# Performance work log

Hardware: AMD Instinct MI355X
Metric: run time of the kernel (lower is better)

## Reference

```python
import jax, jax.numpy as jnp
import numpy as np

HIDDEN = 1024
HEADS = 16
HEAD_DIM = HIDDEN // HEADS  # 64
BLOCK = 1024  # block_size; seq_len > BLOCK triggers ring path
B, S = 1, 4096


def setup_inputs() -> dict:
    key = jax.random.key(0)
    k0, k1, k2, k3, k4 = jax.random.split(key, 5)
    w_scale = 0.02
    return {
        "hidden_states": jax.random.normal(k0, (B, S, HIDDEN), dtype=jnp.float32),
        # weights stored [in, out]; applied as x @ W (equivalent to nn.Linear with W.T)
        "w_q": jax.random.normal(k1, (HIDDEN, HIDDEN), dtype=jnp.float32) * w_scale,
        "w_k": jax.random.normal(k2, (HIDDEN, HIDDEN), dtype=jnp.float32) * w_scale,
        "w_v": jax.random.normal(k3, (HIDDEN, HIDDEN), dtype=jnp.float32) * w_scale,
        "w_o": jax.random.normal(k4, (HIDDEN, HIDDEN), dtype=jnp.float32) * w_scale,
    }


def _ring_attention(q, k, v, block, scale):
    # q,k,v: [B, H, S, D]. Faithful to the torch module: each KV block subtracts
    # its OWN local max (no running-max rescale); exp-sums and weighted-V are
    # accumulated additively across KV blocks, then normalized once at the end.
    b, h, s, d = q.shape
    nb = s // block
    kb = jnp.moveaxis(k.reshape(b, h, nb, block, d), 2, 0)  # [nb, B, H, block, D]
    vb = jnp.moveaxis(v.reshape(b, h, nb, block, d), 2, 0)

    def step(carry, kv):
        num, den = carry
        k_blk, v_blk = kv
        s_blk = jnp.einsum("bhqd,bhkd->bhqk", q, k_blk) * scale  # [B,H,S,block]
        m = jnp.max(s_blk, axis=-1, keepdims=True)               # local max only
        e = jnp.exp(s_blk - m)
        num = num + jnp.einsum("bhqk,bhkd->bhqd", e, v_blk)
        den = den + jnp.sum(e, axis=-1, keepdims=True)
        return (num, den), None

    init = (jnp.zeros_like(q), jnp.zeros((b, h, s, 1), dtype=q.dtype))
    (num, den), _ = jax.lax.scan(step, init, (kb, vb))
    return num / den


def reference(hidden_states, w_q, w_k, w_v, w_o):
    b, s, _ = hidden_states.shape
    q = (hidden_states @ w_q).reshape(b, s, HEADS, HEAD_DIM).transpose(0, 2, 1, 3)
    k = (hidden_states @ w_k).reshape(b, s, HEADS, HEAD_DIM).transpose(0, 2, 1, 3)
    v = (hidden_states @ w_v).reshape(b, s, HEADS, HEAD_DIM).transpose(0, 2, 1, 3)
    scale = HEAD_DIM ** -0.5
    out = _ring_attention(q, k, v, BLOCK, scale)          # [B,H,S,D]
    out = out.transpose(0, 2, 1, 3).reshape(b, s, HIDDEN)  # [B,S,hidden]
    return out @ w_o
```

## Files before the change

kernel.cpp:

```cpp
#include <hip/hip_runtime.h>
#include <hip/hip_bf16.h>

typedef __bf16 bf16;
typedef bf16 bf16x2 __attribute__((ext_vector_type(2)));
typedef bf16 bf16x4 __attribute__((ext_vector_type(4)));
typedef bf16 bf16x8 __attribute__((ext_vector_type(8)));
typedef float f32x4 __attribute__((ext_vector_type(4)));

#define HID 1024
#define NHEADS 16
#define HD 64
#define SEQ 4096

__device__ __forceinline__ void gll16(const void* g, void* l) {
  __builtin_amdgcn_global_load_lds(
      (const __attribute__((address_space(1))) void*)g,
      (__attribute__((address_space(3))) void*)l, 16, 0, 0);
}

__global__ __launch_bounds__(256)
void prep_kernel(const float* __restrict__ X,
                 const float* __restrict__ Wq, const float* __restrict__ Wk,
                 const float* __restrict__ Wv, const float* __restrict__ Wo,
                 bf16* __restrict__ Xb, bf16* __restrict__ Wt)
{
  const int z = blockIdx.z, t = threadIdx.x, bx = blockIdx.x;
  if (z == 0) {
    const float4* src = (const float4*)X;
    const int gid = bx * 256 + t;
    #pragma unroll
    for (int i = 0; i < 16; ++i) {
      float4 v = src[gid + i * 65536];
      bf16x4 o = {(bf16)v.x, (bf16)v.y, (bf16)v.z, (bf16)v.w};
      *(bf16x4*)&Xb[(size_t)(gid + i * 65536) * 4] = o;
    }
  } else {
    const float* W = (z == 1) ? Wq : (z == 2) ? Wk : (z == 3) ? Wv : Wo;
    bf16* dst = Wt + (size_t)(z - 1) * HID * HID;
    const float scale = (z == 1) ? 0.125f : 1.0f;
    __shared__ bf16 T[64][68];
    const int tr = (bx >> 4) * 64, tc = (bx & 15) * 64;
    #pragma unroll
    for (int p = 0; p < 4; ++p) {
      int row = (t >> 4) + p * 16;
      float4 v = *(const float4*)&W[(size_t)(tr + row) * HID + tc + (t & 15) * 4];
      T[row][(t & 15) * 4 + 0] = (bf16)(v.x * scale);
      T[row][(t & 15) * 4 + 1] = (bf16)(v.y * scale);
      T[row][(t & 15) * 4 + 2] = (bf16)(v.z * scale);
      T[row][(t & 15) * 4 + 3] = (bf16)(v.w * scale);
    }
    __syncthreads();
    #pragma unroll
    for (int p = 0; p < 4; ++p) {
      int rp = (t >> 4) + p * 16;
      int cb = (t & 15) * 4;
      bf16x4 o = {T[cb + 0][rp], T[cb + 1][rp], T[cb + 2][rp], T[cb + 3][rp]};
      *(bf16x4*)&dst[(size_t)(tc + rp) * HID + tr + cb] = o;
    }
  }
}

__global__ __launch_bounds__(256)
void qkv_gemm(const bf16* __restrict__ A, const bf16* __restrict__ Wt,
              bf16* __restrict__ Qg, bf16* __restrict__ Kg,
              bf16* __restrict__ Vt)
{
  __shared__ bf16 sbuf[16384];
  bf16* As = sbuf;
  bf16* Bs = sbuf + 8192;

  const int t = threadIdx.x, lane = t & 63, w = t >> 6;
  const int z = blockIdx.z;
  const int n0 = blockIdx.x * 128, m0 = blockIdx.y * 128;
  const bf16* Bt = Wt + (size_t)z * HID * HID;
  const int wm = (w & 1) * 64, wn = (w >> 1) * 64;
  const int fr = lane & 15, quad = lane >> 4;

  f32x4 acc[4][4] = {};

  const int sr = lane >> 3;
  const int sc = ((lane & 7) - sr) & 7;
  const bf16* ga = A  + (size_t)(m0 + w * 32 + sr) * HID + sc * 8;
  const bf16* gb = Bt + (size_t)(n0 + w * 32 + sr) * HID + sc * 8;

  for (int k0 = 0; k0 < HID; k0 += 64) {
    __syncthreads();
    #pragma unroll
    for (int c = 0; c < 4; ++c) {
      gll16(ga + (size_t)(c * 8) * HID + k0, As + (w * 32 + c * 8) * 64);
      gll16(gb + (size_t)(c * 8) * HID + k0, Bs + (w * 32 + c * 8) * 64);
    }
    __syncthreads();
    #pragma unroll
    for (int ks = 0; ks < 2; ++ks) {
      bf16x8 af[4], bg[4];
      #pragma unroll
      for (int i = 0; i < 4; ++i)
        af[i] = *(const bf16x8*)&As[(wm + i * 16 + fr) * 64 +
                                    ((ks * 4 + quad + fr) & 7) * 8];
      #pragma unroll
      for (int i = 0; i < 4; ++i)
        bg[i] = *(const bf16x8*)&Bs[(wn + i * 16 + fr) * 64 +
                                    ((ks * 4 + quad + fr) & 7) * 8];
      #pragma unroll
      for (int mi = 0; mi < 4; ++mi)
        #pragma unroll
        for (int ni = 0; ni < 4; ++ni)
          acc[mi][ni] = __builtin_amdgcn_mfma_f32_16x16x32_bf16(
              af[mi], bg[ni], acc[mi][ni], 0, 0, 0);
    }
  }

  if (z < 2) {
    bf16* C = z ? Kg : Qg;
    #pragma unroll
    for (int mi = 0; mi < 4; ++mi)
      #pragma unroll
      for (int ni = 0; ni < 4; ++ni)
        #pragma unroll
        for (int r = 0; r < 4; ++r)
          C[(size_t)(m0 + wm + mi * 16 + quad * 4 + r) * HID +
            n0 + wn + ni * 16 + fr] = (bf16)acc[mi][ni][r];
  } else {
    __syncthreads();
    #pragma unroll
    for (int mi = 0; mi < 4; ++mi)
      #pragma unroll
      for (int ni = 0; ni < 4; ++ni)
        #pragma unroll
        for (int r = 0; r < 4; ++r) {
          int row = wn + ni * 16 + fr;
          int col = wm + mi * 16 + quad * 4 + r;
          int colS = (col + 8 * (row & 15)) & 127;
          sbuf[row * 128 + colS] = (bf16)acc[mi][ni][r];
        }
    __syncthreads();
    const int row = t >> 1, cb = (t & 1) * 64;
    #pragma unroll
    for (int j = 0; j < 8; ++j) {
      int c0 = (cb + j * 8 + 8 * (row & 15)) & 127;
      *(bf16x8*)&Vt[(size_t)(n0 + row) * SEQ + m0 + cb + j * 8] =
          *(const bf16x8*)&sbuf[row * 128 + c0];
    }
  }
}

__global__ __launch_bounds__(256)
void oproj_gemm(const bf16* __restrict__ A, const bf16* __restrict__ Bt,
                float* __restrict__ C)
{
  __shared__ bf16 sbuf[16384];
  bf16* As = sbuf;
  bf16* Bs = sbuf + 8192;

  const int t = threadIdx.x, lane = t & 63, w = t >> 6;
  const int n0 = blockIdx.x * 128, m0 = blockIdx.y * 128;
  const int wm = (w & 1) * 64, wn = (w >> 1) * 64;
  const int fr = lane & 15, quad = lane >> 4;

  f32x4 acc[4][4] = {};

  const int sr = lane >> 3;
  const int sc = ((lane & 7) - sr) & 7;
  const bf16* ga = A  + (size_t)(m0 + w * 32 + sr) * HID + sc * 8;
  const bf16* gb = Bt + (size_t)(n0 + w * 32 + sr) * HID + sc * 8;

  for (int k0 = 0; k0 < HID; k0 += 64) {
    __syncthreads();
    #pragma unroll
    for (int c = 0; c < 4; ++c) {
      gll16(ga + (size_t)(c * 8) * HID + k0, As + (w * 32 + c * 8) * 64);
      gll16(gb + (size_t)(c * 8) * HID + k0, Bs + (w * 32 + c * 8) * 64);
    }
    __syncthreads();
    #pragma unroll
    for (int ks = 0; ks < 2; ++ks) {
      bf16x8 af[4], bg[4];
      #pragma unroll
      for (int i = 0; i < 4; ++i)
        af[i] = *(const bf16x8*)&As[(wm + i * 16 + fr) * 64 +
                                    ((ks * 4 + quad + fr) & 7) * 8];
      #pragma unroll
      for (int i = 0; i < 4; ++i)
        bg[i] = *(const bf16x8*)&Bs[(wn + i * 16 + fr) * 64 +
                                    ((ks * 4 + quad + fr) & 7) * 8];
      #pragma unroll
      for (int mi = 0; mi < 4; ++mi)
        #pragma unroll
        for (int ni = 0; ni < 4; ++ni)
          acc[mi][ni] = __builtin_amdgcn_mfma_f32_16x16x32_bf16(
              af[mi], bg[ni], acc[mi][ni], 0, 0, 0);
    }
  }

  #pragma unroll
  for (int mi = 0; mi < 4; ++mi)
    #pragma unroll
    for (int ni = 0; ni < 4; ++ni)
      #pragma unroll
      for (int r = 0; r < 4; ++r)
        C[(size_t)(m0 + wm + mi * 16 + quad * 4 + r) * HID +
          n0 + wn + ni * 16 + fr] = acc[mi][ni][r];
}

__global__ __launch_bounds__(256)
void attn3(const bf16* __restrict__ Q, const bf16* __restrict__ K,
           const bf16* __restrict__ Vt, bf16* __restrict__ O)
{
  __shared__ bf16 Ks[2][4096];
  __shared__ bf16 Vs[2][4096];
  __shared__ bf16 Ps[4][2048];

  const int t = threadIdx.x, lane = t & 63, w = t >> 6;
  const int h = blockIdx.y, q0 = blockIdx.x * 128;
  const int fr = lane & 15, quad = lane >> 4;

  bf16x8 bq[2][2];
  #pragma unroll
  for (int qf = 0; qf < 2; ++qf)
    #pragma unroll
    for (int ks = 0; ks < 2; ++ks)
      bq[qf][ks] = *(const bf16x8*)&Q[(size_t)(q0 + w * 32 + qf * 16 + fr) * HID
                                      + h * 64 + ks * 32 + quad * 8];

  const int sr = lane >> 3;
  const int sc = ((lane & 7) - sr) & 7;
  const bf16* gk = K  + (size_t)(w * 16 + sr) * HID + h * 64 + sc * 8;
  const bf16* gv = Vt + (size_t)(h * 64 + w * 16 + sr) * SEQ + sc * 8;

  #pragma unroll
  for (int j = 0; j < 2; ++j) {
    gll16(gk + (size_t)(j * 8) * HID, &Ks[0][(w * 16 + j * 8) * 64]);
    gll16(gv + (size_t)(j * 8) * SEQ, &Vs[0][(w * 16 + j * 8) * 64]);
  }

  f32x4 accN[2][4] = {};
  f32x4 accO[2][4] = {};
  float m_i[2] = {-3e38f, -3e38f}, l_i[2] = {0.f, 0.f}, den[2] = {0.f, 0.f};

  __syncthreads();

  for (int kk = 0; kk < 64; ++kk) {
    const int buf = kk & 1;
    if (kk < 63) {
      const size_t key0n = (size_t)(kk + 1) * 64;
      #pragma unroll
      for (int j = 0; j < 2; ++j) {
        gll16(gk + (key0n + j * 8) * HID, &Ks[buf ^ 1][(w * 16 + j * 8) * 64]);
        gll16(gv + key0n + (size_t)(j * 8) * SEQ,
              &Vs[buf ^ 1][(w * 16 + j * 8) * 64]);
      }
    }

    bf16x8 ak[4][2];
    #pragma unroll
    for (int mt = 0; mt < 4; ++mt)
      #pragma unroll
      for (int ks = 0; ks < 2; ++ks)
        ak[mt][ks] = *(const bf16x8*)&Ks[buf][(mt * 16 + fr) * 64 +
                                             ((ks * 4 + quad + fr) & 7) * 8];

    #pragma unroll
    for (int qf = 0; qf < 2; ++qf) {
      f32x4 s[4];
      #pragma unroll
      for (int mt = 0; mt < 4; ++mt) {
        f32x4 z = {};
        z = __builtin_amdgcn_mfma_f32_16x16x32_bf16(ak[mt][0], bq[qf][0], z, 0, 0, 0);
        z = __builtin_amdgcn_mfma_f32_16x16x32_bf16(ak[mt][1], bq[qf][1], z, 0, 0, 0);
        s[mt] = z;
      }
      float mx = -3e38f;
      #pragma unroll
      for (int mt = 0; mt < 4; ++mt)
        #pragma unroll
        for (int r = 0; r < 4; ++r) mx = fmaxf(mx, s[mt][r]);
      mx = fmaxf(mx, __shfl_xor(mx, 16));
      mx = fmaxf(mx, __shfl_xor(mx, 32));
      const float mnew = fmaxf(m_i[qf], mx);
      const float alpha = __expf(m_i[qf] - mnew);
      m_i[qf] = mnew;
      float sum = 0.f;
      const int prow = (qf * 16 + fr) * 64;
      #pragma unroll
      for (int mt = 0; mt < 4; ++mt) {
        float p0 = __expf(s[mt][0] - mnew);
        float p1 = __expf(s[mt][1] - mnew);
        float p2 = __expf(s[mt][2] - mnew);
        float p3 = __expf(s[mt][3] - mnew);
        sum += (p0 + p1) + (p2 + p3);
        bf16x4 pv = {(bf16)p0, (bf16)p1, (bf16)p2, (bf16)p3};
        *(bf16x4*)&Ps[w][prow + ((mt * 2 + (quad >> 1) + fr) & 7) * 8 +
                         (quad & 1) * 4] = pv;
      }
      sum += __shfl_xor(sum, 16);
      sum += __shfl_xor(sum, 32);
      l_i[qf] = l_i[qf] * alpha + sum;
      #pragma unroll
      for (int dt = 0; dt < 4; ++dt) accO[qf][dt] *= alpha;
    }

    #pragma unroll
    for (int ks = 0; ks < 2; ++ks) {
      bf16x8 bp0 = *(const bf16x8*)&Ps[w][fr * 64 +
                                          ((ks * 4 + quad + fr) & 7) * 8];
      bf16x8 bp1 = *(const bf16x8*)&Ps[w][(16 + fr) * 64 +
                                          ((ks * 4 + quad + fr) & 7) * 8];
      #pragma unroll
      for (int dt = 0; dt < 4; ++dt) {
        bf16x8 av = *(const bf16x8*)&Vs[buf][(dt * 16 + fr) * 64 +
                                            ((ks * 4 + quad + fr) & 7) * 8];
        accO[0][dt] = __builtin_amdgcn_mfma_f32_16x16x32_bf16(av, bp0, accO[0][dt], 0, 0, 0);
        accO[1][dt] = __builtin_amdgcn_mfma_f32_16x16x32_bf16(av, bp1, accO[1][dt], 0, 0, 0);
      }
    }

    if ((kk & 15) == 15) {
      #pragma unroll
      for (int qf = 0; qf < 2; ++qf) {
        #pragma unroll
        for (int dt = 0; dt < 4; ++dt) {
          #pragma unroll
          for (int r = 0; r < 4; ++r) accN[qf][dt][r] += accO[qf][dt][r];
          accO[qf][dt] = (f32x4){0.f, 0.f, 0.f, 0.f};
        }
        den[qf] += l_i[qf];
        l_i[qf] = 0.f;
        m_i[qf] = -3e38f;
      }
    }
    __syncthreads();
  }

  #pragma unroll
  for (int qf = 0; qf < 2; ++qf) {
    const float inv = 1.0f / den[qf];
    const size_t orow = (size_t)(q0 + w * 32 + qf * 16 + fr) * HID + h * 64;
    #pragma unroll
    for (int dt = 0; dt < 4; ++dt) {
      bf16x4 ov = {(bf16)(accN[qf][dt][0] * inv), (bf16)(accN[qf][dt][1] * inv),
                   (bf16)(accN[qf][dt][2] * inv), (bf16)(accN[qf][dt][3] * inv)};
      *(bf16x4*)&O[orow + dt * 16 + quad * 4] = ov;
    }
  }
}

extern "C" void kernel_launch(void* const* d_in, const int* in_sizes, int n_in,
                              void* d_out, int out_size, void* d_ws, size_t ws_size,
                              hipStream_t stream)
{
  const float* X  = (const float*)d_in[0];
  const float* Wq = (const float*)d_in[1];
  const float* Wk = (const float*)d_in[2];
  const float* Wv = (const float*)d_in[3];
  const float* Wo = (const float*)d_in[4];
  float* out = (float*)d_out;

  const size_t MB = 1024 * 1024;
  bf16* Xb  = (bf16*)d_ws;
  bf16* Wt  = (bf16*)((char*)d_ws + 8  * MB);
  bf16* Qg  = (bf16*)((char*)d_ws + 16 * MB);
  bf16* Kg  = (bf16*)((char*)d_ws + 24 * MB);
  bf16* Vtg = (bf16*)((char*)d_ws + 32 * MB);
  bf16* Og  = (bf16*)((char*)d_ws + 40 * MB);

  prep_kernel<<<dim3(256, 1, 5), 256, 0, stream>>>(X, Wq, Wk, Wv, Wo, Xb, Wt);
  qkv_gemm<<<dim3(HID / 128, SEQ / 128, 3), 256, 0, stream>>>(Xb, Wt, Qg, Kg, Vtg);
  attn3<<<dim3(SEQ / 128, NHEADS), 256, 0, stream>>>(Qg, Kg, Vtg, Og);
  oproj_gemm<<<dim3(HID / 128, SEQ / 128), 256, 0, stream>>>(
      Og, Wt + (size_t)3 * HID * HID, out);
}
```

Measured before the change: 274.9 us.

## Split attention KV blocks across grid z with atomic accumulation and normalize pass

Attention is split along the key dimension so each of four z-slices handles one 1024-key block. Partial numerators and denominators are accumulated into fp32 workspace with atomics and then normalized by a separate kernel. The aim is to raise the grid from 512 to 2048 workgroups to fill the GPU better. The cost is a memset, atomic traffic and an extra kernel launch. Double-buffered K/V loading is also replaced by a single buffer with two barriers per iteration, which removes load/compute overlap. Whether the split path runs depends on the workspace being at least 68 MB.

Result: slower. 428.2 us (+55.8%).

```diff
diff --git a/kernel.cpp b/kernel.cpp
--- a/kernel.cpp
+++ b/kernel.cpp
@@ -2,7 +2,6 @@
 #include <hip/hip_bf16.h>
 
 typedef __bf16 bf16;
-typedef bf16 bf16x2 __attribute__((ext_vector_type(2)));
 typedef bf16 bf16x4 __attribute__((ext_vector_type(4)));
 typedef bf16 bf16x8 __attribute__((ext_vector_type(8)));
 typedef float f32x4 __attribute__((ext_vector_type(4)));
@@ -203,16 +202,19 @@
           n0 + wn + ni * 16 + fr] = acc[mi][ni][r];
 }
 
+template <int NSPLIT>
 __global__ __launch_bounds__(256)
-void attn3(const bf16* __restrict__ Q, const bf16* __restrict__ K,
-           const bf16* __restrict__ Vt, bf16* __restrict__ O)
-{
-  __shared__ bf16 Ks[2][4096];
-  __shared__ bf16 Vs[2][4096];
+void attn4(const bf16* __restrict__ Q, const bf16* __restrict__ K,
+           const bf16* __restrict__ Vt, float* __restrict__ numg,
+           float* __restrict__ deng, bf16* __restrict__ Og)
+{
+  __shared__ bf16 Ks[4096];
+  __shared__ bf16 Vs[4096];
   __shared__ bf16 Ps[4][2048];
 
   const int t = threadIdx.x, lane = t & 63, w = t >> 6;
   const int h = blockIdx.y, q0 = blockIdx.x * 128;
+  const int z = blockIdx.z;
   const int fr = lane & 15, quad = lane >> 4;
 
   bf16x8 bq[2][2];
@@ -225,50 +227,44 @@
 
   const int sr = lane >> 3;
   const int sc = ((lane & 7) - sr) & 7;
-  const bf16* gk = K  + (size_t)(w * 16 + sr) * HID + h * 64 + sc * 8;
-  const bf16* gv = Vt + (size_t)(h * 64 + w * 16 + sr) * SEQ + sc * 8;
-
-  #pragma unroll
-  for (int j = 0; j < 2; ++j) {
-    gll16(gk + (size_t)(j * 8) * HID, &Ks[0][(w * 16 + j * 8) * 64]);
-    gll16(gv + (size_t)(j * 8) * SEQ, &Vs[0][(w * 16 + j * 8) * 64]);
-  }
+  const int keybase = z * (4 / NSPLIT) * 1024;
+  const bf16* gk = K  + (size_t)(keybase + w * 16 + sr) * HID + h * 64 + sc * 8;
+  const bf16* gv = Vt + (size_t)(h * 64 + w * 16 + sr) * SEQ + keybase + sc * 8;
 
   f32x4 accN[2][4] = {};
   f32x4 accO[2][4] = {};
-  float m_i[2] = {-3e38f, -3e38f}, l_i[2] = {0.f, 0.f}, den[2] = {0.f, 0.f};
-
-  __syncthreads();
-
-  for (int kk = 0; kk < 64; ++kk) {
-    const int buf = kk & 1;
-    if (kk < 63) {
-      const size_t key0n = (size_t)(kk + 1) * 64;
+  float m_i[2] = {-3e38f, -3e38f}, l_i[2] = {0.f, 0.f}, dsum[2] = {0.f, 0.f};
+
+  const int NIT = (4 / NSPLIT) * 16;
+  for (int kk = 0; kk < NIT; ++kk) {
+    __syncthreads();
+    {
+      const size_t key0 = (size_t)kk * 64;
       #pragma unroll
       for (int j = 0; j < 2; ++j) {
-        gll16(gk + (key0n + j * 8) * HID, &Ks[buf ^ 1][(w * 16 + j * 8) * 64]);
-        gll16(gv + key0n + (size_t)(j * 8) * SEQ,
-              &Vs[buf ^ 1][(w * 16 + j * 8) * 64]);
-      }
-    }
+        gll16(gk + (key0 + j * 8) * HID, &Ks[(w * 16 + j * 8) * 64]);
+        gll16(gv + key0 + (size_t)(j * 8) * SEQ, &Vs[(w * 16 + j * 8) * 64]);
+      }
+    }
+    __syncthreads();
 
     bf16x8 ak[4][2];
     #pragma unroll
     for (int mt = 0; mt < 4; ++mt)
       #pragma unroll
       for (int ks = 0; ks < 2; ++ks)
-        ak[mt][ks] = *(const bf16x8*)&Ks[buf][(mt * 16 + fr) * 64 +
-                                             ((ks * 4 + quad + fr) & 7) * 8];
+        ak[mt][ks] = *(const bf16x8*)&Ks[(mt * 16 + fr) * 64 +
+                                         ((ks * 4 + quad + fr) & 7) * 8];
 
     #pragma unroll
     for (int qf = 0; qf < 2; ++qf) {
       f32x4 s[4];
       #pragma unroll
       for (int mt = 0; mt < 4; ++mt) {
-        f32x4 z = {};
-        z = __builtin_amdgcn_mfma_f32_16x16x32_bf16(ak[mt][0], bq[qf][0], z, 0, 0, 0);
-        z = __builtin_amdgcn_mfma_f32_16x16x32_bf16(ak[mt][1], bq[qf][1], z, 0, 0, 0);
-        s[mt] = z;
+        f32x4 zz = {};
+        zz = __builtin_amdgcn_mfma_f32_16x16x32_bf16(ak[mt][0], bq[qf][0], zz, 0, 0, 0);
+        zz = __builtin_amdgcn_mfma_f32_16x16x32_bf16(ak[mt][1], bq[qf][1], zz, 0, 0, 0);
+        s[mt] = zz;
       }
       float mx = -3e38f;
       #pragma unroll
@@ -308,8 +304,8 @@
                                           ((ks * 4 + quad + fr) & 7) * 8];
       #pragma unroll
       for (int dt = 0; dt < 4; ++dt) {
-        bf16x8 av = *(const bf16x8*)&Vs[buf][(dt * 16 + fr) * 64 +
-                                            ((ks * 4 + quad + fr) & 7) * 8];
+        bf16x8 av = *(const bf16x8*)&Vs[(dt * 16 + fr) * 64 +
+                                        ((ks * 4 + quad + fr) & 7) * 8];
         accO[0][dt] = __builtin_amdgcn_mfma_f32_16x16x32_bf16(av, bp0, accO[0][dt], 0, 0, 0);
         accO[1][dt] = __builtin_amdgcn_mfma_f32_16x16x32_bf16(av, bp1, accO[1][dt], 0, 0, 0);
       }
@@ -324,25 +320,55 @@
           for (int r = 0; r < 4; ++r) accN[qf][dt][r] += accO[qf][dt][r];
           accO[qf][dt] = (f32x4){0.f, 0.f, 0.f, 0.f};
         }
-        den[qf] += l_i[qf];
+        dsum[qf] += l_i[qf];
         l_i[qf] = 0.f;
         m_i[qf] = -3e38f;
       }
     }
-    __syncthreads();
-  }
-
-  #pragma unroll
-  for (int qf = 0; qf < 2; ++qf) {
-    const float inv = 1.0f / den[qf];
-    const size_t orow = (size_t)(q0 + w * 32 + qf * 16 + fr) * HID + h * 64;
-    #pragma unroll
-    for (int dt = 0; dt < 4; ++dt) {
-      bf16x4 ov = {(bf16)(accN[qf][dt][0] * inv), (bf16)(accN[qf][dt][1] * inv),
-                   (bf16)(accN[qf][dt][2] * inv), (bf16)(accN[qf][dt][3] * inv)};
-      *(bf16x4*)&O[orow + dt * 16 + quad * 4] = ov;
-    }
-  }
+  }
+
+  if (NSPLIT == 1) {
+    #pragma unroll
+    for (int qf = 0; qf < 2; ++qf) {
+      const float inv = 1.0f / dsum[qf];
+      const size_t orow = (size_t)(q0 + w * 32 + qf * 16 + fr) * HID + h * 64;
+      #pragma unroll
+      for (int dt = 0; dt < 4; ++dt) {
+        bf16x4 ov = {(bf16)(accN[qf][dt][0] * inv), (bf16)(accN[qf][dt][1] * inv),
+                     (bf16)(accN[qf][dt][2] * inv), (bf16)(accN[qf][dt][3] * inv)};
+        *(bf16x4*)&Og[orow + dt * 16 + quad * 4] = ov;
+      }
+    }
+  } else {
+    #pragma unroll
+    for (int qf = 0; qf < 2; ++qf) {
+      const int qrow = q0 + w * 32 + qf * 16 + fr;
+      const size_t orow = (size_t)qrow * HID + h * 64;
+      #pragma unroll
+      for (int dt = 0; dt < 4; ++dt) {
+        #pragma unroll
+        for (int r = 0; r < 4; ++r)
+          atomicAdd(&numg[orow + dt * 16 + quad * 4 + r], accN[qf][dt][r]);
+      }
+      if (quad == 0) atomicAdd(&deng[qrow * NHEADS + h], dsum[qf]);
+    }
+  }
+}
+
+__global__ __launch_bounds__(256)
+void norm_kernel(const float* __restrict__ numg, const float* __restrict__ deng,
+                 bf16* __restrict__ Og)
+{
+  const int gid = blockIdx.x * 256 + threadIdx.x;
+  const size_t base = (size_t)gid * 8;
+  const int q = (int)(base >> 10), c = (int)(base & 1023), h = c >> 6;
+  const float inv = 1.0f / deng[q * NHEADS + h];
+  float4 a = *(const float4*)&numg[base];
+  float4 b = *(const float4*)&numg[base + 4];
+  bf16x8 o = {(bf16)(a.x * inv), (bf16)(a.y * inv), (bf16)(a.z * inv),
+              (bf16)(a.w * inv), (bf16)(b.x * inv), (bf16)(b.y * inv),
+              (bf16)(b.z * inv), (bf16)(b.w * inv)};
+  *(bf16x8*)&Og[base] = o;
 }
 
 extern "C" void kernel_launch(void* const* d_in, const int* in_sizes, int n_in,
@@ -357,16 +383,32 @@
   float* out = (float*)d_out;
 
   const size_t MB = 1024 * 1024;
-  bf16* Xb  = (bf16*)d_ws;
-  bf16* Wt  = (bf16*)((char*)d_ws + 8  * MB);
-  bf16* Qg  = (bf16*)((char*)d_ws + 16 * MB);
-  bf16* Kg  = (bf16*)((char*)d_ws + 24 * MB);
-  bf16* Vtg = (bf16*)((char*)d_ws + 32 * MB);
-  bf16* Og  = (bf16*)((char*)d_ws + 40 * MB);
+  bf16*  Xb   = (bf16*)d_ws;
+  bf16*  Wt   = (bf16*)((char*)d_ws + 8  * MB);
+  bf16*  Qg   = (bf16*)((char*)d_ws + 16 * MB);
+  bf16*  Kg   = (bf16*)((char*)d_ws + 24 * MB);
+  bf16*  Vtg  = (bf16*)((char*)d_ws + 32 * MB);
+  float* numg = (float*)((char*)d_ws + 40 * MB);
+  float* deng = (float*)((char*)d_ws + 56 * MB);
+  bf16*  OgS  = (bf16*)((char*)d_ws + 57 * MB);
+  bf16*  OgF  = (bf16*)((char*)d_ws + 40 * MB);
 
   prep_kernel<<<dim3(256, 1, 5), 256, 0, stream>>>(X, Wq, Wk, Wv, Wo, Xb, Wt);
   qkv_gemm<<<dim3(HID / 128, SEQ / 128, 3), 256, 0, stream>>>(Xb, Wt, Qg, Kg, Vtg);
-  attn3<<<dim3(SEQ / 128, NHEADS), 256, 0, stream>>>(Qg, Kg, Vtg, Og);
-  oproj_gemm<<<dim3(HID / 128, SEQ / 128), 256, 0, stream>>>(
-      Og, Wt + (size_t)3 * HID * HID, out);
-}
+
+  const bool split = ws_size >= 68 * MB;
+  if (split) {
+    hipMemsetAsync((char*)d_ws + 40 * MB, 0,
+                   (size_t)SEQ * HID * 4 + (size_t)SEQ * NHEADS * 4, stream);
+    attn4<4><<<dim3(SEQ / 128, NHEADS, 4), 256, 0, stream>>>(
+        Qg, Kg, Vtg, numg, deng, nullptr);
+    norm_kernel<<<(SEQ * HID) / (256 * 8), 256, 0, stream>>>(numg, deng, OgS);
+    oproj_gemm<<<dim3(HID / 128, SEQ / 128), 256, 0, stream>>>(
+        OgS, Wt + (size_t)3 * HID * HID, out);
+  } else {
+    attn4<1><<<dim3(SEQ / 128, NHEADS, 1), 256, 0, stream>>>(
+        Qg, Kg, Vtg, nullptr, nullptr, OgF);
+    oproj_gemm<<<dim3(HID / 128, SEQ / 128), 256, 0, stream>>>(
+        OgF, Wt + (size_t)3 * HID * HID, out);
+  }
+}
```

## Split attention KV range across two wave groups with LDS merge

Applied to the files above, without the earlier changes.

The attention kernel now launches 512 threads per block, and two halves of four waves each process half of the key sequence for the same 128 queries. Their partial numerators and denominators are merged through shared memory at the end. This doubles the waves per query tile to hide latency and shortens the serial KV loop. In exchange it drops the double-buffered prefetch, so each iteration now loads and then syncs, and it uses more LDS per block, which may reduce occupancy. The output buffer is also moved to reuse the X workspace.

New measurement: 282.5 us. +2.8%, slower.

```diff
diff --git a/kernel.cpp b/kernel.cpp
--- a/kernel.cpp
+++ b/kernel.cpp
@@ -2,7 +2,6 @@
 #include <hip/hip_bf16.h>
 
 typedef __bf16 bf16;
-typedef bf16 bf16x2 __attribute__((ext_vector_type(2)));
 typedef bf16 bf16x4 __attribute__((ext_vector_type(4)));
 typedef bf16 bf16x8 __attribute__((ext_vector_type(8)));
 typedef float f32x4 __attribute__((ext_vector_type(4)));
@@ -203,72 +202,68 @@
           n0 + wn + ni * 16 + fr] = acc[mi][ni][r];
 }
 
-__global__ __launch_bounds__(256)
-void attn3(const bf16* __restrict__ Q, const bf16* __restrict__ K,
-           const bf16* __restrict__ Vt, bf16* __restrict__ O)
-{
-  __shared__ bf16 Ks[2][4096];
-  __shared__ bf16 Vs[2][4096];
-  __shared__ bf16 Ps[4][2048];
+__global__ __launch_bounds__(512)
+void attn5(const bf16* __restrict__ Q, const bf16* __restrict__ K,
+           const bf16* __restrict__ Vt, bf16* __restrict__ Og)
+{
+  __shared__ __align__(16) char pool[67584];
 
   const int t = threadIdx.x, lane = t & 63, w = t >> 6;
+  const int half = w >> 2, wl = w & 3;
   const int h = blockIdx.y, q0 = blockIdx.x * 128;
   const int fr = lane & 15, quad = lane >> 4;
+
+  bf16* Kl = (bf16*)pool + half * 8192;
+  bf16* Vl = Kl + 4096;
+  bf16* Pw = (bf16*)(pool + 32768) + w * 2048;
 
   bf16x8 bq[2][2];
   #pragma unroll
   for (int qf = 0; qf < 2; ++qf)
     #pragma unroll
     for (int ks = 0; ks < 2; ++ks)
-      bq[qf][ks] = *(const bf16x8*)&Q[(size_t)(q0 + w * 32 + qf * 16 + fr) * HID
+      bq[qf][ks] = *(const bf16x8*)&Q[(size_t)(q0 + wl * 32 + qf * 16 + fr) * HID
                                       + h * 64 + ks * 32 + quad * 8];
 
   const int sr = lane >> 3;
   const int sc = ((lane & 7) - sr) & 7;
-  const bf16* gk = K  + (size_t)(w * 16 + sr) * HID + h * 64 + sc * 8;
-  const bf16* gv = Vt + (size_t)(h * 64 + w * 16 + sr) * SEQ + sc * 8;
-
-  #pragma unroll
-  for (int j = 0; j < 2; ++j) {
-    gll16(gk + (size_t)(j * 8) * HID, &Ks[0][(w * 16 + j * 8) * 64]);
-    gll16(gv + (size_t)(j * 8) * SEQ, &Vs[0][(w * 16 + j * 8) * 64]);
-  }
+  const int keybase = half * 2048;
+  const bf16* gk = K  + (size_t)(keybase + wl * 16 + sr) * HID + h * 64 + sc * 8;
+  const bf16* gv = Vt + (size_t)(h * 64 + wl * 16 + sr) * SEQ + keybase + sc * 8;
 
   f32x4 accN[2][4] = {};
   f32x4 accO[2][4] = {};
-  float m_i[2] = {-3e38f, -3e38f}, l_i[2] = {0.f, 0.f}, den[2] = {0.f, 0.f};
-
-  __syncthreads();
-
-  for (int kk = 0; kk < 64; ++kk) {
-    const int buf = kk & 1;
-    if (kk < 63) {
-      const size_t key0n = (size_t)(kk + 1) * 64;
+  float m_i[2] = {-3e38f, -3e38f}, l_i[2] = {0.f, 0.f}, dsum[2] = {0.f, 0.f};
+
+  for (int kk = 0; kk < 32; ++kk) {
+    __syncthreads();
+    {
+      const size_t key0 = (size_t)kk * 64;
       #pragma unroll
       for (int j = 0; j < 2; ++j) {
-        gll16(gk + (key0n + j * 8) * HID, &Ks[buf ^ 1][(w * 16 + j * 8) * 64]);
-        gll16(gv + key0n + (size_t)(j * 8) * SEQ,
-              &Vs[buf ^ 1][(w * 16 + j * 8) * 64]);
-      }
-    }
+        gll16(gk + (key0 + j * 8) * HID, Kl + (wl * 16 + j * 8) * 64);
+        gll16(gv + key0 + (size_t)(j * 8) * SEQ, Vl + (wl * 16 + j * 8) * 64);
+      }
+    }
+    __syncthreads();
 
     bf16x8 ak[4][2];
     #pragma unroll
     for (int mt = 0; mt < 4; ++mt)
       #pragma unroll
       for (int ks = 0; ks < 2; ++ks)
-        ak[mt][ks] = *(const bf16x8*)&Ks[buf][(mt * 16 + fr) * 64 +
-                                             ((ks * 4 + quad + fr) & 7) * 8];
+        ak[mt][ks] = *(const bf16x8*)&Kl[(mt * 16 + fr) * 64 +
+                                         ((ks * 4 + quad + fr) & 7) * 8];
 
     #pragma unroll
     for (int qf = 0; qf < 2; ++qf) {
       f32x4 s[4];
       #pragma unroll
       for (int mt = 0; mt < 4; ++mt) {
-        f32x4 z = {};
-        z = __builtin_amdgcn_mfma_f32_16x16x32_bf16(ak[mt][0], bq[qf][0], z, 0, 0, 0);
-        z = __builtin_amdgcn_mfma_f32_16x16x32_bf16(ak[mt][1], bq[qf][1], z, 0, 0, 0);
-        s[mt] = z;
+        f32x4 zz = {};
+        zz = __builtin_amdgcn_mfma_f32_16x16x32_bf16(ak[mt][0], bq[qf][0], zz, 0, 0, 0);
+        zz = __builtin_amdgcn_mfma_f32_16x16x32_bf16(ak[mt][1], bq[qf][1], zz, 0, 0, 0);
+        s[mt] = zz;
       }
       float mx = -3e38f;
       #pragma unroll
@@ -290,8 +285,8 @@
         float p3 = __expf(s[mt][3] - mnew);
         sum += (p0 + p1) + (p2 + p3);
         bf16x4 pv = {(bf16)p0, (bf16)p1, (bf16)p2, (bf16)p3};
-        *(bf16x4*)&Ps[w][prow + ((mt * 2 + (quad >> 1) + fr) & 7) * 8 +
-                         (quad & 1) * 4] = pv;
+        *(bf16x4*)&Pw[prow + ((mt * 2 + (quad >> 1) + fr) & 7) * 8 +
+                      (quad & 1) * 4] = pv;
       }
       sum += __shfl_xor(sum, 16);
       sum += __shfl_xor(sum, 32);
@@ -302,14 +297,13 @@
 
     #pragma unroll
     for (int ks = 0; ks < 2; ++ks) {
-      bf16x8 bp0 = *(const bf16x8*)&Ps[w][fr * 64 +
-                                          ((ks * 4 + quad + fr) & 7) * 8];
-      bf16x8 bp1 = *(const bf16x8*)&Ps[w][(16 + fr) * 64 +
-                                          ((ks * 4 + quad + fr) & 7) * 8];
+      bf16x8 bp0 = *(const bf16x8*)&Pw[fr * 64 + ((ks * 4 + quad + fr) & 7) * 8];
+      bf16x8 bp1 = *(const bf16x8*)&Pw[(16 + fr) * 64 +
+                                       ((ks * 4 + quad + fr) & 7) * 8];
       #pragma unroll
       for (int dt = 0; dt < 4; ++dt) {
-        bf16x8 av = *(const bf16x8*)&Vs[buf][(dt * 16 + fr) * 64 +
-                                            ((ks * 4 + quad + fr) & 7) * 8];
+        bf16x8 av = *(const bf16x8*)&Vl[(dt * 16 + fr) * 64 +
+                                        ((ks * 4 + quad + fr) & 7) * 8];
         accO[0][dt] = __builtin_amdgcn_mfma_f32_16x16x32_bf16(av, bp0, accO[0][dt], 0, 0, 0);
         accO[1][dt] = __builtin_amdgcn_mfma_f32_16x16x32_bf16(av, bp1, accO[1][dt], 0, 0, 0);
       }
@@ -324,23 +318,44 @@
           for (int r = 0; r < 4; ++r) accN[qf][dt][r] += accO[qf][dt][r];
           accO[qf][dt] = (f32x4){0.f, 0.f, 0.f, 0.f};
         }
-        den[qf] += l_i[qf];
+        dsum[qf] += l_i[qf];
         l_i[qf] = 0.f;
         m_i[qf] = -3e38f;
       }
     }
-    __syncthreads();
-  }
-
-  #pragma unroll
-  for (int qf = 0; qf < 2; ++qf) {
-    const float inv = 1.0f / den[qf];
-    const size_t orow = (size_t)(q0 + w * 32 + qf * 16 + fr) * HID + h * 64;
-    #pragma unroll
-    for (int dt = 0; dt < 4; ++dt) {
-      bf16x4 ov = {(bf16)(accN[qf][dt][0] * inv), (bf16)(accN[qf][dt][1] * inv),
-                   (bf16)(accN[qf][dt][2] * inv), (bf16)(accN[qf][dt][3] * inv)};
-      *(bf16x4*)&O[orow + dt * 16 + quad * 4] = ov;
+  }
+
+  __syncthreads();
+  float* scr = (float*)(pool + 32768);
+  float* dS  = (float*)(pool + 65536);
+  if (half == 1) {
+    #pragma unroll
+    for (int qf = 0; qf < 2; ++qf) {
+      #pragma unroll
+      for (int dt = 0; dt < 4; ++dt)
+        #pragma unroll
+        for (int r = 0; r < 4; ++r)
+          scr[(qf * 16 + dt * 4 + r) * 256 + wl * 64 + lane] = accN[qf][dt][r];
+      if (quad == 0) dS[wl * 32 + qf * 16 + fr] = dsum[qf];
+    }
+  }
+  __syncthreads();
+  if (half == 0) {
+    #pragma unroll
+    for (int qf = 0; qf < 2; ++qf) {
+      const float dtot = dsum[qf] + dS[wl * 32 + qf * 16 + fr];
+      const float inv = 1.0f / dtot;
+      const size_t orow = (size_t)(q0 + wl * 32 + qf * 16 + fr) * HID + h * 64;
+      #pragma unroll
+      for (int dt = 0; dt < 4; ++dt) {
+        float v0 = accN[qf][dt][0] + scr[(qf * 16 + dt * 4 + 0) * 256 + wl * 64 + lane];
+        float v1 = accN[qf][dt][1] + scr[(qf * 16 + dt * 4 + 1) * 256 + wl * 64 + lane];
+        float v2 = accN[qf][dt][2] + scr[(qf * 16 + dt * 4 + 2) * 256 + wl * 64 + lane];
+        float v3 = accN[qf][dt][3] + scr[(qf * 16 + dt * 4 + 3) * 256 + wl * 64 + lane];
+        bf16x4 ov = {(bf16)(v0 * inv), (bf16)(v1 * inv),
+                     (bf16)(v2 * inv), (bf16)(v3 * inv)};
+        *(bf16x4*)&Og[orow + dt * 16 + quad * 4] = ov;
+      }
     }
   }
 }
@@ -362,11 +377,11 @@
   bf16* Qg  = (bf16*)((char*)d_ws + 16 * MB);
   bf16* Kg  = (bf16*)((char*)d_ws + 24 * MB);
   bf16* Vtg = (bf16*)((char*)d_ws + 32 * MB);
-  bf16* Og  = (bf16*)((char*)d_ws + 40 * MB);
+  bf16* Og  = (bf16*)d_ws;
 
   prep_kernel<<<dim3(256, 1, 5), 256, 0, stream>>>(X, Wq, Wk, Wv, Wo, Xb, Wt);
   qkv_gemm<<<dim3(HID / 128, SEQ / 128, 3), 256, 0, stream>>>(Xb, Wt, Qg, Kg, Vtg);
-  attn3<<<dim3(SEQ / 128, NHEADS), 256, 0, stream>>>(Qg, Kg, Vtg, Og);
+  attn5<<<dim3(SEQ / 128, NHEADS), 512, 0, stream>>>(Qg, Kg, Vtg, Og);
   oproj_gemm<<<dim3(HID / 128, SEQ / 128), 256, 0, stream>>>(
       Og, Wt + (size_t)3 * HID * HID, out);
 }
```
